# Kernel tuning notes

Measured on AMD Instinct MI355X. Metric: run time of the kernel, lower is better.

Reference implementation:

```python
import jax, jax.numpy as jnp
import numpy as np

T, D, H, P, HEADS, EC = 16, 192, 128, 128, 4, 32  # EC = proj_dim // 4
HD = P // HEADS  # head dim = 32


def setup_inputs() -> dict:
    key = jax.random.key(0)
    ks = jax.random.split(key, 16)
    def nrm(k, shp, s=0.02):
        return jax.random.normal(k, shp, jnp.float32) * s
    x = jax.random.normal(ks[0], (T, H, D), jnp.float32)
    u = jax.random.uniform(ks[1], (D, D))
    w = jax.random.uniform(ks[2], (D, D))
    edge_w = jnp.where(u < 0.05, w, 0.0)
    return dict(
        x=x, edge_w=edge_w,
        W_node=nrm(ks[3], (H, P)), b_node=jnp.zeros(P),
        W_edge=nrm(ks[4], (1, EC)), b_edge=jnp.zeros(EC),
        time_enc=nrm(ks[5], (P,)),
        Wqkv=nrm(ks[6], (P, 3 * P)), bqkv=jnp.zeros(3 * P),
        Wo=nrm(ks[7], (P, P)), bo=jnp.zeros(P),
        W1=nrm(ks[8], (P, 4 * P)), b1=jnp.zeros(4 * P),
        W2=nrm(ks[9], (4 * P, P)), b2=jnp.zeros(P),
        g1=jnp.ones(P), beta1=jnp.zeros(P), g2=jnp.ones(P), beta2=jnp.zeros(P),
        Wc1=nrm(ks[10], (2 * P + EC, P)), bc1=jnp.zeros(P),
        Wc2=nrm(ks[11], (P, 1)), bc2=jnp.zeros(1),
        Wd1=nrm(ks[12], (2 * P, P)), bd1=jnp.zeros(P),
        Wd2=nrm(ks[13], (P, 1)), bd2=jnp.zeros(1),
    )


def _ln(z, g, b):
    m = z.mean(-1, keepdims=True)
    v = ((z - m) ** 2).mean(-1, keepdims=True)
    return (z - m) / jnp.sqrt(v + 1e-5) * g + b


def _heads(t, S):
    return t.reshape(S, HEADS, HD).transpose(1, 0, 2)  # (h, S, hd)


def _forward(x, edge_w, W_node, b_node, W_edge, b_edge, time_enc, Wqkv, bqkv,
             Wo, bo, W1, b1, W2, b2, g1, beta1, g2, beta2,
             Wc1, bc1, Wc2, bc2, Wd1, bd1, Wd2, bd2):
    S = T * D
    # node encoder: (T,H,D) -> (T,D,H) -> (T*D,H) -> (T*D,P), dropout is eval-mode identity
    xf = x.transpose(0, 2, 1).reshape(S, H)
    h = jax.nn.relu(xf @ W_node + b_node)
    # learned time encoding scaled by time index
    t_idx = jnp.repeat(jnp.arange(T, dtype=jnp.float32), D)
    h = h + time_enc[None, :] * t_idx[:, None]
    # spatiotemporal mask: attend to self+neighbors at t and t-1 (vectorized kron)
    adj = (edge_w > 0) | jnp.eye(D, dtype=bool)
    time_allow = jnp.eye(T, dtype=bool) | jnp.eye(T, k=-1, dtype=bool)
    allow = (time_allow[:, None, :, None] & adj[None, :, None, :]).reshape(S, S)
    scale = 1.0 / np.sqrt(HD)
    z = h
    for _ in range(2):  # num_layers=2, shared weights as in the source
        y = _ln(z, g1, beta1)
        qkv = y @ Wqkv + bqkv
        q, k, v = jnp.split(qkv, 3, axis=-1)
        scores = jnp.einsum('hqd,hkd->hqk', _heads(q, S), _heads(k, S)) * scale
        scores = jnp.where(allow[None], scores, -jnp.inf)
        a = jax.nn.softmax(scores, axis=-1)
        attn = jnp.einsum('hqk,hkd->hqd', a, _heads(v, S))
        z = z + attn.transpose(1, 0, 2).reshape(S, P) @ Wo + bo
        y = _ln(z, g2, beta2)
        z = z + jax.nn.relu(y @ W1 + b1) @ W2 + b2
    nf = z.reshape(T, D, P)
    curr, nxt = nf[:-1], nf[1:]  # (T-1, D, P)
    # edge encoder: Linear(1->EC)+ReLU on edge weights
    edge_enc = jax.nn.relu(edge_w[:, :, None] * W_edge[0] + b_edge)  # (D, D, EC)
    # update classifier on concat[next_i, curr_j, edge] -> split the first matmul
    hn = nxt @ Wc1[:P]            # (T-1, D, P)
    hc = curr @ Wc1[P:2 * P]      # (T-1, D, P)
    he = edge_enc @ Wc1[2 * P:]   # (D, D, P)
    hcls = jax.nn.relu(hn[:, :, None, :] + hc[:, None, :, :] + he[None] + bc1)
    logits = (hcls @ Wc2)[..., 0] + bc2[0]  # (T-1, D, D)
    mask = (edge_w == 0) & ~jnp.eye(D, dtype=bool)
    logits = jnp.where(mask[None], -1e9, logits)
    # distance predictor on concat[curr, next]
    hd = jax.nn.relu(curr @ Wd1[:P] + nxt @ Wd1[P:] + bd1)
    dist = (hd @ Wd2)[..., 0] + bd2[0]  # (T-1, D)
    return logits, dist


def reference(x, edge_w, W_node, b_node, W_edge, b_edge, time_enc, Wqkv, bqkv,
              Wo, bo, W1, b1, W2, b2, g1, beta1, g2, beta2,
              Wc1, bc1, Wc2, bc2, Wd1, bd1, Wd2, bd2):
    return _forward(x, edge_w, W_node, b_node, W_edge, b_edge, time_enc, Wqkv,
                    bqkv, Wo, bo, W1, b1, W2, b2, g1, beta1, g2, beta2,
                    Wc1, bc1, Wc2, bc2, Wd1, bd1, Wd2, bd2)
```

## Files before the change

kernel.cpp:

```cpp
#include <hip/hip_runtime.h>
#include <hip/hip_bf16.h>

constexpr int T_ = 16;
constexpr int D_ = 192;
constexpr int H_ = 128;
constexpr int P_ = 128;
constexpr int HEADS_ = 4;
constexpr int HD_ = 32;
constexpr int EC_ = 32;
constexpr int S_ = T_ * D_;
constexpr int FF_ = 512;
constexpr float SCALE_ = 0.17677669529663687f;

__global__ __launch_bounds__(64) void adj_kernel(const float* __restrict__ edge_w,
                                                 int* __restrict__ adj_cnt,
                                                 int* __restrict__ adj_list) {
  int i = blockIdx.x;
  int lane = threadIdx.x;
  int cnt = 0;
  for (int base = 0; base < D_; base += 64) {
    int j = base + lane;
    bool pred = (edge_w[i * D_ + j] > 0.f) || (j == i);
    unsigned long long mb = __ballot(pred);
    int ofs = __popcll(mb & ((1ull << lane) - 1ull));
    if (pred) adj_list[i * D_ + cnt + ofs] = j;
    cnt += __popcll(mb);
  }
  if (lane == 0) adj_cnt[i] = cnt;
}

__global__ __launch_bounds__(128) void node_embed_kernel(
    const float* __restrict__ x, const float* __restrict__ W_node,
    const float* __restrict__ b_node, const float* __restrict__ time_enc,
    float* __restrict__ z) {
  int s0 = blockIdx.x * 8;
  int j = threadIdx.x;
  __shared__ float As[8 * H_];
  for (int idx = j; idx < 8 * H_; idx += 128) {
    int r = idx >> 7;
    int h = idx & 127;
    int s = s0 + r;
    int t = s / D_;
    int d = s - t * D_;
    As[idx] = x[(t * H_ + h) * D_ + d];
  }
  __syncthreads();
  float acc[8];
  float bj = b_node[j];
#pragma unroll
  for (int r = 0; r < 8; ++r) acc[r] = bj;
  for (int h = 0; h < H_; h += 4) {
    float4 w;
    w.x = W_node[(h + 0) * P_ + j];
    w.y = W_node[(h + 1) * P_ + j];
    w.z = W_node[(h + 2) * P_ + j];
    w.w = W_node[(h + 3) * P_ + j];
#pragma unroll
    for (int r = 0; r < 8; ++r) {
      const float4 a = *reinterpret_cast<const float4*>(&As[r * H_ + h]);
      acc[r] = fmaf(a.x, w.x, acc[r]);
      acc[r] = fmaf(a.y, w.y, acc[r]);
      acc[r] = fmaf(a.z, w.z, acc[r]);
      acc[r] = fmaf(a.w, w.w, acc[r]);
    }
  }
  float te = time_enc[j];
#pragma unroll
  for (int r = 0; r < 8; ++r) {
    int s = s0 + r;
    int t = s / D_;
    z[s * P_ + j] = fmaxf(acc[r], 0.f) + te * (float)t;
  }
}

template <int K, int N, int NT, int BM, bool RELU, bool ACCUM, bool BIAS, bool LN>
__global__ __launch_bounds__(NT) void gemm2_k(
    const float* __restrict__ A, const float* __restrict__ B,
    const float* __restrict__ bias, const float* __restrict__ lng,
    const float* __restrict__ lnb, float* __restrict__ C) {
  constexpr int CPT = N / NT;
  int m0 = blockIdx.x * BM;
  int tid = threadIdx.x;
  __shared__ float As[BM * K];
  {
    float4* As4 = reinterpret_cast<float4*>(As);
    const float4* A4 = reinterpret_cast<const float4*>(A + (size_t)m0 * K);
    for (int idx = tid; idx < BM * K / 4; idx += NT) As4[idx] = A4[idx];
  }
  __syncthreads();
  if (LN) {
    static_assert(!LN || K == 128, "LN requires K==128");
    int wv = tid >> 6, lane = tid & 63;
    constexpr int NW = NT / 64;
    for (int r = wv; r < BM; r += NW) {
      float v0 = As[r * K + lane], v1 = As[r * K + 64 + lane];
      float s = v0 + v1;
#pragma unroll
      for (int m = 1; m < 64; m <<= 1) s += __shfl_xor(s, m);
      float mean = s * (1.f / 128.f);
      float d0 = v0 - mean, d1 = v1 - mean;
      float q = d0 * d0 + d1 * d1;
#pragma unroll
      for (int m = 1; m < 64; m <<= 1) q += __shfl_xor(q, m);
      float inv = 1.f / sqrtf(q * (1.f / 128.f) + 1e-5f);
      As[r * K + lane] = d0 * inv * lng[lane] + lnb[lane];
      As[r * K + 64 + lane] = d1 * inv * lng[lane + 64] + lnb[lane + 64];
    }
    __syncthreads();
  }

  if (CPT == 2) {
    int c0 = 2 * tid;
    float acc0[BM], acc1[BM];
    float b0 = BIAS ? bias[c0] : 0.f;
    float b1 = BIAS ? bias[c0 + 1] : 0.f;
#pragma unroll
    for (int r = 0; r < BM; ++r) {
      acc0[r] = b0;
      acc1[r] = b1;
    }
    for (int k = 0; k < K; k += 4) {
      float2 bv0 = *reinterpret_cast<const float2*>(B + (size_t)(k + 0) * N + c0);
      float2 bv1 = *reinterpret_cast<const float2*>(B + (size_t)(k + 1) * N + c0);
      float2 bv2 = *reinterpret_cast<const float2*>(B + (size_t)(k + 2) * N + c0);
      float2 bv3 = *reinterpret_cast<const float2*>(B + (size_t)(k + 3) * N + c0);
#pragma unroll
      for (int r = 0; r < BM; ++r) {
        const float4 a = *reinterpret_cast<const float4*>(&As[r * K + k]);
        acc0[r] = fmaf(a.x, bv0.x, acc0[r]);
        acc1[r] = fmaf(a.x, bv0.y, acc1[r]);
        acc0[r] = fmaf(a.y, bv1.x, acc0[r]);
        acc1[r] = fmaf(a.y, bv1.y, acc1[r]);
        acc0[r] = fmaf(a.z, bv2.x, acc0[r]);
        acc1[r] = fmaf(a.z, bv2.y, acc1[r]);
        acc0[r] = fmaf(a.w, bv3.x, acc0[r]);
        acc1[r] = fmaf(a.w, bv3.y, acc1[r]);
      }
    }
#pragma unroll
    for (int r = 0; r < BM; ++r) {
      float v0 = acc0[r], v1 = acc1[r];
      if (RELU) {
        v0 = fmaxf(v0, 0.f);
        v1 = fmaxf(v1, 0.f);
      }
      float* cp = C + (size_t)(m0 + r) * N + c0;
      if (ACCUM) {
        float2 old = *reinterpret_cast<float2*>(cp);
        old.x += v0;
        old.y += v1;
        *reinterpret_cast<float2*>(cp) = old;
      } else {
        float2 nv;
        nv.x = v0;
        nv.y = v1;
        *reinterpret_cast<float2*>(cp) = nv;
      }
    }
  } else {
    int j = tid;
    float acc[BM];
    float bj = BIAS ? bias[j] : 0.f;
#pragma unroll
    for (int r = 0; r < BM; ++r) acc[r] = bj;
    for (int k = 0; k < K; k += 4) {
      float b0 = B[(size_t)(k + 0) * N + j];
      float b1 = B[(size_t)(k + 1) * N + j];
      float b2 = B[(size_t)(k + 2) * N + j];
      float b3 = B[(size_t)(k + 3) * N + j];
#pragma unroll
      for (int r = 0; r < BM; ++r) {
        const float4 a = *reinterpret_cast<const float4*>(&As[r * K + k]);
        acc[r] = fmaf(a.x, b0, acc[r]);
        acc[r] = fmaf(a.y, b1, acc[r]);
        acc[r] = fmaf(a.z, b2, acc[r]);
        acc[r] = fmaf(a.w, b3, acc[r]);
      }
    }
#pragma unroll
    for (int r = 0; r < BM; ++r) {
      float v = acc[r];
      if (RELU) v = fmaxf(v, 0.f);
      float* cp = C + (size_t)(m0 + r) * N + j;
      if (ACCUM)
        *cp += v;
      else
        *cp = v;
    }
  }
}

__global__ __launch_bounds__(256) void pre_gemm_kernel(
    const float* __restrict__ A, const float* __restrict__ Wc1,
    const float* __restrict__ Wd1, float* __restrict__ pre) {
  constexpr int K = 128, N = 512, NT = 256, BM = 8;
  int m0 = blockIdx.x * BM;
  int tid = threadIdx.x;
  __shared__ float As[BM * K];
  {
    float4* As4 = reinterpret_cast<float4*>(As);
    const float4* A4 = reinterpret_cast<const float4*>(A + (size_t)m0 * K);
    for (int idx = tid; idx < BM * K / 4; idx += NT) As4[idx] = A4[idx];
  }
  __syncthreads();
  int c0 = 2 * tid;
  int seg = c0 >> 7;
  int cc = c0 & 127;
  const float* Bbase = (seg < 2 ? Wc1 : Wd1) + ((seg & 1) ? 128 * P_ : 0) + cc;
  float acc0[BM], acc1[BM];
#pragma unroll
  for (int r = 0; r < BM; ++r) {
    acc0[r] = 0.f;
    acc1[r] = 0.f;
  }
  for (int k = 0; k < K; k += 4) {
    float2 bv0 = *reinterpret_cast<const float2*>(Bbase + (size_t)(k + 0) * P_);
    float2 bv1 = *reinterpret_cast<const float2*>(Bbase + (size_t)(k + 1) * P_);
    float2 bv2 = *reinterpret_cast<const float2*>(Bbase + (size_t)(k + 2) * P_);
    float2 bv3 = *reinterpret_cast<const float2*>(Bbase + (size_t)(k + 3) * P_);
#pragma unroll
    for (int r = 0; r < BM; ++r) {
      const float4 a = *reinterpret_cast<const float4*>(&As[r * K + k]);
      acc0[r] = fmaf(a.x, bv0.x, acc0[r]);
      acc1[r] = fmaf(a.x, bv0.y, acc1[r]);
      acc0[r] = fmaf(a.y, bv1.x, acc0[r]);
      acc1[r] = fmaf(a.y, bv1.y, acc1[r]);
      acc0[r] = fmaf(a.z, bv2.x, acc0[r]);
      acc1[r] = fmaf(a.z, bv2.y, acc1[r]);
      acc0[r] = fmaf(a.w, bv3.x, acc0[r]);
      acc1[r] = fmaf(a.w, bv3.y, acc1[r]);
    }
  }
#pragma unroll
  for (int r = 0; r < BM; ++r) {
    float2 nv;
    nv.x = acc0[r];
    nv.y = acc1[r];
    *reinterpret_cast<float2*>(pre + (size_t)(m0 + r) * N + c0) = nv;
  }
}

__global__ __launch_bounds__(128) void attn_kernel(
    const float* __restrict__ qkv, const int* __restrict__ adj_cnt,
    const int* __restrict__ adj_list, float* __restrict__ out) {
  int s = blockIdx.x;
  int t = s / D_, d1 = s - t * D_;
  int tid = threadIdx.x;
  __shared__ int klist[D_];
  __shared__ float scores[HEADS_][2 * D_];

  int nd2 = adj_cnt[d1];
  for (int kd = tid; kd < nd2; kd += 128) klist[kd] = adj_list[d1 * D_ + kd];
  __syncthreads();
  int t0 = (t > 0) ? t - 1 : 0;
  int ntp = (t > 0) ? 2 : 1;
  int nk = nd2 * ntp;

  float q = qkv[s * 384 + tid];
  int h = tid >> 5, dd = tid & 31;

  for (int tp = 0; tp < ntp; ++tp) {
    int tt = t0 + tp;
    for (int kd = 0; kd < nd2; ++kd) {
      int sk = tt * D_ + klist[kd];
      float partial = q * qkv[sk * 384 + P_ + tid];
      partial += __shfl_xor(partial, 1);
      partial += __shfl_xor(partial, 2);
      partial += __shfl_xor(partial, 4);
      partial += __shfl_xor(partial, 8);
      partial += __shfl_xor(partial, 16);
      if (dd == 0) scores[h][tp * nd2 + kd] = partial * SCALE_;
    }
  }
  __syncthreads();

  float mx = -1e30f;
  for (int ki = dd; ki < nk; ki += 32) mx = fmaxf(mx, scores[h][ki]);
  mx = fmaxf(mx, __shfl_xor(mx, 1));
  mx = fmaxf(mx, __shfl_xor(mx, 2));
  mx = fmaxf(mx, __shfl_xor(mx, 4));
  mx = fmaxf(mx, __shfl_xor(mx, 8));
  mx = fmaxf(mx, __shfl_xor(mx, 16));
  float ssum = 0.f;
  for (int ki = dd; ki < nk; ki += 32) {
    float e = expf(scores[h][ki] - mx);
    scores[h][ki] = e;
    ssum += e;
  }
  ssum += __shfl_xor(ssum, 1);
  ssum += __shfl_xor(ssum, 2);
  ssum += __shfl_xor(ssum, 4);
  ssum += __shfl_xor(ssum, 8);
  ssum += __shfl_xor(ssum, 16);
  float inv = 1.f / ssum;
  __syncthreads();

  float acc = 0.f;
  for (int tp = 0; tp < ntp; ++tp) {
    int tt = t0 + tp;
    for (int kd = 0; kd < nd2; ++kd) {
      float aev = scores[h][tp * nd2 + kd];
      int sk = tt * D_ + klist[kd];
      acc = fmaf(aev, qkv[sk * 384 + 2 * P_ + tid], acc);
    }
  }
  out[s * P_ + tid] = acc * inv;
}

__global__ __launch_bounds__(64) void logits_kernel(
    const float* __restrict__ pre, const int* __restrict__ adj_cnt,
    const int* __restrict__ adj_list, const float* __restrict__ edge_w,
    const float* __restrict__ W_edge, const float* __restrict__ b_edge,
    const float* __restrict__ Wc1e, const float* __restrict__ bc1,
    const float* __restrict__ Wc2, const float* __restrict__ bc2,
    float* __restrict__ logits) {
  int i = blockIdx.x;
  int t = blockIdx.y;
  int lane = threadIdx.x;
  float* lrow = logits + (size_t)(t * D_ + i) * D_;
  for (int j = lane; j < D_; j += 64) lrow[j] = -1e9f;

  const float* hnr = pre + (size_t)((t + 1) * D_ + i) * 512;
  float hn0 = hnr[lane], hn1 = hnr[lane + 64];
  float bc1_0 = bc1[lane], bc1_1 = bc1[lane + 64];
  float wc0 = Wc2[lane], wc1 = Wc2[lane + 64];
  float bb = bc2[0];
  int cnt = adj_cnt[i];
  for (int jj = 0; jj < cnt; ++jj) {
    int j = adj_list[i * D_ + jj];
    float w = edge_w[i * D_ + j];
    float he0 = 0.f, he1 = 0.f;
#pragma unroll 8
    for (int e = 0; e < EC_; ++e) {
      float enc = fmaxf(fmaf(w, W_edge[e], b_edge[e]), 0.f);
      he0 = fmaf(enc, Wc1e[e * P_ + lane], he0);
      he1 = fmaf(enc, Wc1e[e * P_ + lane + 64], he1);
    }
    const float* hcr = pre + (size_t)(t * D_ + j) * 512 + 128;
    float sacc = fmaxf(hn0 + hcr[lane] + he0 + bc1_0, 0.f) * wc0 +
                 fmaxf(hn1 + hcr[lane + 64] + he1 + bc1_1, 0.f) * wc1;
#pragma unroll
    for (int m = 1; m < 64; m <<= 1) sacc += __shfl_xor(sacc, m);
    if (lane == 0) lrow[j] = sacc + bb;
  }
}

__global__ __launch_bounds__(256) void dist_kernel(
    const float* __restrict__ pre, const float* __restrict__ bd1,
    const float* __restrict__ Wd2, const float* __restrict__ bd2,
    float* __restrict__ dist) {
  int row = blockIdx.x * 4 + (threadIdx.x >> 6);
  int lane = threadIdx.x & 63;
  const float* a = pre + (size_t)row * 512 + 256;
  const float* b = pre + (size_t)(row + D_) * 512 + 384;
  float v0 = fmaxf(a[lane] + b[lane] + bd1[lane], 0.f) * Wd2[lane];
  float v1 = fmaxf(a[lane + 64] + b[lane + 64] + bd1[lane + 64], 0.f) * Wd2[lane + 64];
  float s = v0 + v1;
#pragma unroll
  for (int m = 1; m < 64; m <<= 1) s += __shfl_xor(s, m);
  if (lane == 0) dist[row] = s + bd2[0];
}

extern "C" void kernel_launch(void* const* d_in, const int* in_sizes, int n_in,
                              void* d_out, int out_size, void* d_ws,
                              size_t ws_size, hipStream_t stream) {
  const float* x = (const float*)d_in[0];
  const float* edge_w = (const float*)d_in[1];
  const float* W_node = (const float*)d_in[2];
  const float* b_node = (const float*)d_in[3];
  const float* W_edge = (const float*)d_in[4];
  const float* b_edge = (const float*)d_in[5];
  const float* time_enc = (const float*)d_in[6];
  const float* Wqkv = (const float*)d_in[7];
  const float* bqkv = (const float*)d_in[8];
  const float* Wo = (const float*)d_in[9];
  const float* bo = (const float*)d_in[10];
  const float* W1 = (const float*)d_in[11];
  const float* b1 = (const float*)d_in[12];
  const float* W2 = (const float*)d_in[13];
  const float* b2 = (const float*)d_in[14];
  const float* g1 = (const float*)d_in[15];
  const float* beta1 = (const float*)d_in[16];
  const float* g2 = (const float*)d_in[17];
  const float* beta2 = (const float*)d_in[18];
  const float* Wc1 = (const float*)d_in[19];
  const float* bc1 = (const float*)d_in[20];
  const float* Wc2 = (const float*)d_in[21];
  const float* bc2 = (const float*)d_in[22];
  const float* Wd1 = (const float*)d_in[23];
  const float* bd1 = (const float*)d_in[24];
  const float* Wd2 = (const float*)d_in[25];
  const float* bd2 = (const float*)d_in[26];

  float* ws = (float*)d_ws;
  float* qkvb = ws;
  float* attnout = qkvb + S_ * 3 * P_;
  float* mid = attnout + S_ * P_;
  float* z = mid + S_ * FF_;
  int* adj_cnt = (int*)(z + S_ * P_);
  int* adj_list = adj_cnt + D_;
  float* pre = mid;

  float* logits = (float*)d_out;
  float* dist = (float*)d_out + (T_ - 1) * D_ * D_;

  adj_kernel<<<D_, 64, 0, stream>>>(edge_w, adj_cnt, adj_list);
  node_embed_kernel<<<S_ / 8, 128, 0, stream>>>(x, W_node, b_node, time_enc, z);

  for (int it = 0; it < 2; ++it) {
    gemm2_k<128, 384, 192, 8, false, false, true, true>
        <<<S_ / 8, 192, 0, stream>>>(z, Wqkv, bqkv, g1, beta1, qkvb);
    attn_kernel<<<S_, 128, 0, stream>>>(qkvb, adj_cnt, adj_list, attnout);
    gemm2_k<128, 128, 128, 8, false, true, true, false>
        <<<S_ / 8, 128, 0, stream>>>(attnout, Wo, bo, nullptr, nullptr, z);
    gemm2_k<128, 512, 256, 8, true, false, true, true>
        <<<S_ / 8, 256, 0, stream>>>(z, W1, b1, g2, beta2, mid);
    gemm2_k<512, 128, 128, 8, false, true, true, false>
        <<<S_ / 8, 128, 0, stream>>>(mid, W2, b2, nullptr, nullptr, z);
  }

  pre_gemm_kernel<<<S_ / 8, 256, 0, stream>>>(z, Wc1, Wd1, pre);

  logits_kernel<<<dim3(D_, T_ - 1), 64, 0, stream>>>(
      pre, adj_cnt, adj_list, edge_w, W_edge, b_edge, Wc1 + 2 * P_ * P_, bc1,
      Wc2, bc2, logits);
  dist_kernel<<<(T_ - 1) * D_ / 4, 256, 0, stream>>>(pre, bd1, Wd2, bd2, dist);
}
```

Baseline: 356.1 us.

## Fuse transformer layer stages into fewer kernels and drop intermediate buffers

The adjacency build is folded into the node-embedding kernel, and the Wo projection plus residual add into the attention kernel. The two FFN matmuls become one kernel that keeps the hidden activations in shared memory, and the dist head is merged into the logits kernel. The QKV kernel now processes 16 rows per block, and two barriers in attention are removed because each head's scores are produced and consumed by lanes of one wavefront. The goal is fewer launches and less global-memory traffic for attnout and mid. In exchange, the Wo projection now runs one row per block with little weight reuse, and the large shared-memory footprint of the FFN kernel may lower occupancy.

```diff
diff --git a/kernel.cpp b/kernel.cpp
--- a/kernel.cpp
+++ b/kernel.cpp
@@ -1,226 +1,116 @@
 #include <hip/hip_runtime.h>
-#include <hip/hip_bf16.h>
 
 constexpr int T_ = 16;
 constexpr int D_ = 192;
 constexpr int H_ = 128;
 constexpr int P_ = 128;
-constexpr int HEADS_ = 4;
-constexpr int HD_ = 32;
 constexpr int EC_ = 32;
 constexpr int S_ = T_ * D_;
 constexpr int FF_ = 512;
 constexpr float SCALE_ = 0.17677669529663687f;
 
-__global__ __launch_bounds__(64) void adj_kernel(const float* __restrict__ edge_w,
-                                                 int* __restrict__ adj_cnt,
-                                                 int* __restrict__ adj_list) {
-  int i = blockIdx.x;
-  int lane = threadIdx.x;
-  int cnt = 0;
-  for (int base = 0; base < D_; base += 64) {
-    int j = base + lane;
-    bool pred = (edge_w[i * D_ + j] > 0.f) || (j == i);
-    unsigned long long mb = __ballot(pred);
-    int ofs = __popcll(mb & ((1ull << lane) - 1ull));
-    if (pred) adj_list[i * D_ + cnt + ofs] = j;
-    cnt += __popcll(mb);
-  }
-  if (lane == 0) adj_cnt[i] = cnt;
-}
-
-__global__ __launch_bounds__(128) void node_embed_kernel(
+__device__ __forceinline__ float wave_sum64(float v) {
+#pragma unroll
+  for (int m = 1; m < 64; m <<= 1) v += __shfl_xor(v, m);
+  return v;
+}
+
+__global__ __launch_bounds__(128) void embed_adj_kernel(
     const float* __restrict__ x, const float* __restrict__ W_node,
     const float* __restrict__ b_node, const float* __restrict__ time_enc,
-    float* __restrict__ z) {
-  int s0 = blockIdx.x * 8;
-  int j = threadIdx.x;
+    const float* __restrict__ edge_w, float* __restrict__ z,
+    int* __restrict__ adj_cnt, int* __restrict__ adj_list) {
+  int bx = blockIdx.x;
+  int tid = threadIdx.x;
+  if (bx < D_ && tid < 64) {
+    int lane = tid, cnt = 0;
+    for (int base = 0; base < D_; base += 64) {
+      int j = base + lane;
+      bool pred = (edge_w[bx * D_ + j] > 0.f) || (j == bx);
+      unsigned long long mb = __ballot(pred);
+      int ofs = __popcll(mb & ((1ull << lane) - 1ull));
+      if (pred) adj_list[bx * D_ + cnt + ofs] = j;
+      cnt += __popcll(mb);
+    }
+    if (lane == 0) adj_cnt[bx] = cnt;
+  }
   __shared__ float As[8 * H_];
-  for (int idx = j; idx < 8 * H_; idx += 128) {
-    int r = idx >> 7;
-    int h = idx & 127;
-    int s = s0 + r;
-    int t = s / D_;
-    int d = s - t * D_;
+  int m0 = bx * 8;
+  for (int idx = tid; idx < 8 * H_; idx += 128) {
+    int r = idx >> 7, h = idx & 127;
+    int s = m0 + r, t = s / D_, d = s - t * D_;
     As[idx] = x[(t * H_ + h) * D_ + d];
   }
   __syncthreads();
+  int j = tid;
   float acc[8];
   float bj = b_node[j];
 #pragma unroll
   for (int r = 0; r < 8; ++r) acc[r] = bj;
   for (int h = 0; h < H_; h += 4) {
-    float4 w;
-    w.x = W_node[(h + 0) * P_ + j];
-    w.y = W_node[(h + 1) * P_ + j];
-    w.z = W_node[(h + 2) * P_ + j];
-    w.w = W_node[(h + 3) * P_ + j];
+    float w0 = W_node[(h + 0) * P_ + j], w1 = W_node[(h + 1) * P_ + j];
+    float w2 = W_node[(h + 2) * P_ + j], w3 = W_node[(h + 3) * P_ + j];
 #pragma unroll
     for (int r = 0; r < 8; ++r) {
       const float4 a = *reinterpret_cast<const float4*>(&As[r * H_ + h]);
-      acc[r] = fmaf(a.x, w.x, acc[r]);
-      acc[r] = fmaf(a.y, w.y, acc[r]);
-      acc[r] = fmaf(a.z, w.z, acc[r]);
-      acc[r] = fmaf(a.w, w.w, acc[r]);
+      acc[r] = fmaf(a.x, w0, acc[r]);
+      acc[r] = fmaf(a.y, w1, acc[r]);
+      acc[r] = fmaf(a.z, w2, acc[r]);
+      acc[r] = fmaf(a.w, w3, acc[r]);
     }
   }
   float te = time_enc[j];
 #pragma unroll
   for (int r = 0; r < 8; ++r) {
-    int s = s0 + r;
-    int t = s / D_;
-    z[s * P_ + j] = fmaxf(acc[r], 0.f) + te * (float)t;
-  }
-}
-
-template <int K, int N, int NT, int BM, bool RELU, bool ACCUM, bool BIAS, bool LN>
-__global__ __launch_bounds__(NT) void gemm2_k(
-    const float* __restrict__ A, const float* __restrict__ B,
-    const float* __restrict__ bias, const float* __restrict__ lng,
-    const float* __restrict__ lnb, float* __restrict__ C) {
-  constexpr int CPT = N / NT;
+    int s = m0 + r;
+    z[(size_t)s * P_ + j] = fmaxf(acc[r], 0.f) + te * (float)(s / D_);
+  }
+}
+
+__global__ __launch_bounds__(192) void qkv_kernel(
+    const float* __restrict__ z, const float* __restrict__ Wqkv,
+    const float* __restrict__ bqkv, const float* __restrict__ g,
+    const float* __restrict__ b, float* __restrict__ qkvb) {
+  constexpr int BM = 16, NT = 192, N = 384;
   int m0 = blockIdx.x * BM;
   int tid = threadIdx.x;
-  __shared__ float As[BM * K];
-  {
-    float4* As4 = reinterpret_cast<float4*>(As);
-    const float4* A4 = reinterpret_cast<const float4*>(A + (size_t)m0 * K);
-    for (int idx = tid; idx < BM * K / 4; idx += NT) As4[idx] = A4[idx];
-  }
-  __syncthreads();
-  if (LN) {
-    static_assert(!LN || K == 128, "LN requires K==128");
+  __shared__ float As[BM * 128];
+  {
+    float4* As4 = (float4*)As;
+    const float4* Z4 = (const float4*)(z + (size_t)m0 * 128);
+    for (int idx = tid; idx < BM * 32; idx += NT) As4[idx] = Z4[idx];
+  }
+  __syncthreads();
+  {
     int wv = tid >> 6, lane = tid & 63;
-    constexpr int NW = NT / 64;
-    for (int r = wv; r < BM; r += NW) {
-      float v0 = As[r * K + lane], v1 = As[r * K + 64 + lane];
-      float s = v0 + v1;
-#pragma unroll
-      for (int m = 1; m < 64; m <<= 1) s += __shfl_xor(s, m);
+    for (int r = wv; r < BM; r += 3) {
+      float v0 = As[r * 128 + lane], v1 = As[r * 128 + 64 + lane];
+      float s = wave_sum64(v0 + v1);
       float mean = s * (1.f / 128.f);
       float d0 = v0 - mean, d1 = v1 - mean;
-      float q = d0 * d0 + d1 * d1;
-#pragma unroll
-      for (int m = 1; m < 64; m <<= 1) q += __shfl_xor(q, m);
+      float q = wave_sum64(d0 * d0 + d1 * d1);
       float inv = 1.f / sqrtf(q * (1.f / 128.f) + 1e-5f);
-      As[r * K + lane] = d0 * inv * lng[lane] + lnb[lane];
-      As[r * K + 64 + lane] = d1 * inv * lng[lane + 64] + lnb[lane + 64];
-    }
-    __syncthreads();
-  }
-
-  if (CPT == 2) {
-    int c0 = 2 * tid;
-    float acc0[BM], acc1[BM];
-    float b0 = BIAS ? bias[c0] : 0.f;
-    float b1 = BIAS ? bias[c0 + 1] : 0.f;
+      As[r * 128 + lane] = d0 * inv * g[lane] + b[lane];
+      As[r * 128 + 64 + lane] = d1 * inv * g[lane + 64] + b[lane + 64];
+    }
+  }
+  __syncthreads();
+  int c0 = 2 * tid;
+  float acc0[BM], acc1[BM];
+  float b0c = bqkv[c0], b1c = bqkv[c0 + 1];
+#pragma unroll
+  for (int r = 0; r < BM; ++r) {
+    acc0[r] = b0c;
+    acc1[r] = b1c;
+  }
+  for (int k = 0; k < 128; k += 4) {
+    float2 bv0 = *(const float2*)(Wqkv + (size_t)(k + 0) * N + c0);
+    float2 bv1 = *(const float2*)(Wqkv + (size_t)(k + 1) * N + c0);
+    float2 bv2 = *(const float2*)(Wqkv + (size_t)(k + 2) * N + c0);
+    float2 bv3 = *(const float2*)(Wqkv + (size_t)(k + 3) * N + c0);
 #pragma unroll
     for (int r = 0; r < BM; ++r) {
-      acc0[r] = b0;
-      acc1[r] = b1;
-    }
-    for (int k = 0; k < K; k += 4) {
-      float2 bv0 = *reinterpret_cast<const float2*>(B + (size_t)(k + 0) * N + c0);
-      float2 bv1 = *reinterpret_cast<const float2*>(B + (size_t)(k + 1) * N + c0);
-      float2 bv2 = *reinterpret_cast<const float2*>(B + (size_t)(k + 2) * N + c0);
-      float2 bv3 = *reinterpret_cast<const float2*>(B + (size_t)(k + 3) * N + c0);
-#pragma unroll
-      for (int r = 0; r < BM; ++r) {
-        const float4 a = *reinterpret_cast<const float4*>(&As[r * K + k]);
-        acc0[r] = fmaf(a.x, bv0.x, acc0[r]);
-        acc1[r] = fmaf(a.x, bv0.y, acc1[r]);
-        acc0[r] = fmaf(a.y, bv1.x, acc0[r]);
-        acc1[r] = fmaf(a.y, bv1.y, acc1[r]);
-        acc0[r] = fmaf(a.z, bv2.x, acc0[r]);
-        acc1[r] = fmaf(a.z, bv2.y, acc1[r]);
-        acc0[r] = fmaf(a.w, bv3.x, acc0[r]);
-        acc1[r] = fmaf(a.w, bv3.y, acc1[r]);
-      }
-    }
-#pragma unroll
-    for (int r = 0; r < BM; ++r) {
-      float v0 = acc0[r], v1 = acc1[r];
-      if (RELU) {
-        v0 = fmaxf(v0, 0.f);
-        v1 = fmaxf(v1, 0.f);
-      }
-      float* cp = C + (size_t)(m0 + r) * N + c0;
-      if (ACCUM) {
-        float2 old = *reinterpret_cast<float2*>(cp);
-        old.x += v0;
-        old.y += v1;
-        *reinterpret_cast<float2*>(cp) = old;
-      } else {
-        float2 nv;
-        nv.x = v0;
-        nv.y = v1;
-        *reinterpret_cast<float2*>(cp) = nv;
-      }
-    }
-  } else {
-    int j = tid;
-    float acc[BM];
-    float bj = BIAS ? bias[j] : 0.f;
-#pragma unroll
-    for (int r = 0; r < BM; ++r) acc[r] = bj;
-    for (int k = 0; k < K; k += 4) {
-      float b0 = B[(size_t)(k + 0) * N + j];
-      float b1 = B[(size_t)(k + 1) * N + j];
-      float b2 = B[(size_t)(k + 2) * N + j];
-      float b3 = B[(size_t)(k + 3) * N + j];
-#pragma unroll
-      for (int r = 0; r < BM; ++r) {
-        const float4 a = *reinterpret_cast<const float4*>(&As[r * K + k]);
-        acc[r] = fmaf(a.x, b0, acc[r]);
-        acc[r] = fmaf(a.y, b1, acc[r]);
-        acc[r] = fmaf(a.z, b2, acc[r]);
-        acc[r] = fmaf(a.w, b3, acc[r]);
-      }
-    }
-#pragma unroll
-    for (int r = 0; r < BM; ++r) {
-      float v = acc[r];
-      if (RELU) v = fmaxf(v, 0.f);
-      float* cp = C + (size_t)(m0 + r) * N + j;
-      if (ACCUM)
-        *cp += v;
-      else
-        *cp = v;
-    }
-  }
-}
-
-__global__ __launch_bounds__(256) void pre_gemm_kernel(
-    const float* __restrict__ A, const float* __restrict__ Wc1,
-    const float* __restrict__ Wd1, float* __restrict__ pre) {
-  constexpr int K = 128, N = 512, NT = 256, BM = 8;
-  int m0 = blockIdx.x * BM;
-  int tid = threadIdx.x;
-  __shared__ float As[BM * K];
-  {
-    float4* As4 = reinterpret_cast<float4*>(As);
-    const float4* A4 = reinterpret_cast<const float4*>(A + (size_t)m0 * K);
-    for (int idx = tid; idx < BM * K / 4; idx += NT) As4[idx] = A4[idx];
-  }
-  __syncthreads();
-  int c0 = 2 * tid;
-  int seg = c0 >> 7;
-  int cc = c0 & 127;
-  const float* Bbase = (seg < 2 ? Wc1 : Wd1) + ((seg & 1) ? 128 * P_ : 0) + cc;
-  float acc0[BM], acc1[BM];
-#pragma unroll
-  for (int r = 0; r < BM; ++r) {
-    acc0[r] = 0.f;
-    acc1[r] = 0.f;
-  }
-  for (int k = 0; k < K; k += 4) {
-    float2 bv0 = *reinterpret_cast<const float2*>(Bbase + (size_t)(k + 0) * P_);
-    float2 bv1 = *reinterpret_cast<const float2*>(Bbase + (size_t)(k + 1) * P_);
-    float2 bv2 = *reinterpret_cast<const float2*>(Bbase + (size_t)(k + 2) * P_);
-    float2 bv3 = *reinterpret_cast<const float2*>(Bbase + (size_t)(k + 3) * P_);
-#pragma unroll
-    for (int r = 0; r < BM; ++r) {
-      const float4 a = *reinterpret_cast<const float4*>(&As[r * K + k]);
+      const float4 a = *(const float4*)&As[r * 128 + k];
       acc0[r] = fmaf(a.x, bv0.x, acc0[r]);
       acc1[r] = fmaf(a.x, bv0.y, acc1[r]);
       acc0[r] = fmaf(a.y, bv1.x, acc0[r]);
@@ -236,18 +126,20 @@
     float2 nv;
     nv.x = acc0[r];
     nv.y = acc1[r];
-    *reinterpret_cast<float2*>(pre + (size_t)(m0 + r) * N + c0) = nv;
-  }
-}
-
-__global__ __launch_bounds__(128) void attn_kernel(
-    const float* __restrict__ qkv, const int* __restrict__ adj_cnt,
-    const int* __restrict__ adj_list, float* __restrict__ out) {
+    *(float2*)(qkvb + (size_t)(m0 + r) * N + c0) = nv;
+  }
+}
+
+__global__ __launch_bounds__(128) void attn_wo_kernel(
+    const float* __restrict__ qkvb, const int* __restrict__ adj_cnt,
+    const int* __restrict__ adj_list, const float* __restrict__ Wo,
+    const float* __restrict__ bo, float* __restrict__ z) {
   int s = blockIdx.x;
   int t = s / D_, d1 = s - t * D_;
   int tid = threadIdx.x;
   __shared__ int klist[D_];
-  __shared__ float scores[HEADS_][2 * D_];
+  __shared__ float scores[4][2 * D_];
+  __shared__ float att[128];
 
   int nd2 = adj_cnt[d1];
   for (int kd = tid; kd < nd2; kd += 128) klist[kd] = adj_list[d1 * D_ + kd];
@@ -256,14 +148,14 @@
   int ntp = (t > 0) ? 2 : 1;
   int nk = nd2 * ntp;
 
-  float q = qkv[s * 384 + tid];
+  float q = qkvb[(size_t)s * 384 + tid];
   int h = tid >> 5, dd = tid & 31;
 
   for (int tp = 0; tp < ntp; ++tp) {
     int tt = t0 + tp;
     for (int kd = 0; kd < nd2; ++kd) {
       int sk = tt * D_ + klist[kd];
-      float partial = q * qkv[sk * 384 + P_ + tid];
+      float partial = q * qkvb[(size_t)sk * 384 + P_ + tid];
       partial += __shfl_xor(partial, 1);
       partial += __shfl_xor(partial, 2);
       partial += __shfl_xor(partial, 4);
@@ -272,8 +164,6 @@
       if (dd == 0) scores[h][tp * nd2 + kd] = partial * SCALE_;
     }
   }
-  __syncthreads();
-
   float mx = -1e30f;
   for (int ki = dd; ki < nk; ki += 32) mx = fmaxf(mx, scores[h][ki]);
   mx = fmaxf(mx, __shfl_xor(mx, 1));
@@ -293,7 +183,6 @@
   ssum += __shfl_xor(ssum, 8);
   ssum += __shfl_xor(ssum, 16);
   float inv = 1.f / ssum;
-  __syncthreads();
 
   float acc = 0.f;
   for (int tp = 0; tp < ntp; ++tp) {
@@ -301,23 +190,176 @@
     for (int kd = 0; kd < nd2; ++kd) {
       float aev = scores[h][tp * nd2 + kd];
       int sk = tt * D_ + klist[kd];
-      acc = fmaf(aev, qkv[sk * 384 + 2 * P_ + tid], acc);
-    }
-  }
-  out[s * P_ + tid] = acc * inv;
-}
-
-__global__ __launch_bounds__(64) void logits_kernel(
+      acc = fmaf(aev, qkvb[(size_t)sk * 384 + 2 * P_ + tid], acc);
+    }
+  }
+  att[tid] = acc * inv;
+  __syncthreads();
+
+  int c = tid;
+  float p = 0.f;
+  for (int k = 0; k < 128; k += 4) {
+    const float4 a = *(const float4*)&att[k];
+    p = fmaf(a.x, Wo[(size_t)(k + 0) * P_ + c], p);
+    p = fmaf(a.y, Wo[(size_t)(k + 1) * P_ + c], p);
+    p = fmaf(a.z, Wo[(size_t)(k + 2) * P_ + c], p);
+    p = fmaf(a.w, Wo[(size_t)(k + 3) * P_ + c], p);
+  }
+  z[(size_t)s * P_ + c] += p + bo[c];
+}
+
+__global__ __launch_bounds__(256) void ffn_kernel(
+    const float* __restrict__ zin, const float* __restrict__ W1,
+    const float* __restrict__ b1, const float* __restrict__ W2,
+    const float* __restrict__ b2, const float* __restrict__ g,
+    const float* __restrict__ b, float* __restrict__ z) {
+  constexpr int BM = 8, NT = 256;
+  int m0 = blockIdx.x * BM;
+  int tid = threadIdx.x;
+  __shared__ float As[BM * 128];
+  __shared__ float mid[BM * FF_];
+  {
+    float4* As4 = (float4*)As;
+    const float4* Z4 = (const float4*)(zin + (size_t)m0 * 128);
+    for (int idx = tid; idx < BM * 32; idx += NT) As4[idx] = Z4[idx];
+  }
+  __syncthreads();
+  {
+    int wv = tid >> 6, lane = tid & 63;
+    for (int r = wv; r < BM; r += 4) {
+      float v0 = As[r * 128 + lane], v1 = As[r * 128 + 64 + lane];
+      float s = wave_sum64(v0 + v1);
+      float mean = s * (1.f / 128.f);
+      float d0 = v0 - mean, d1 = v1 - mean;
+      float qv = wave_sum64(d0 * d0 + d1 * d1);
+      float inv = 1.f / sqrtf(qv * (1.f / 128.f) + 1e-5f);
+      As[r * 128 + lane] = d0 * inv * g[lane] + b[lane];
+      As[r * 128 + 64 + lane] = d1 * inv * g[lane + 64] + b[lane + 64];
+    }
+  }
+  __syncthreads();
+  {
+    int c0 = 2 * tid;
+    float acc0[BM], acc1[BM];
+    float bb0 = b1[c0], bb1 = b1[c0 + 1];
+#pragma unroll
+    for (int r = 0; r < BM; ++r) {
+      acc0[r] = bb0;
+      acc1[r] = bb1;
+    }
+    for (int k = 0; k < 128; k += 4) {
+      float2 bv0 = *(const float2*)(W1 + (size_t)(k + 0) * FF_ + c0);
+      float2 bv1 = *(const float2*)(W1 + (size_t)(k + 1) * FF_ + c0);
+      float2 bv2 = *(const float2*)(W1 + (size_t)(k + 2) * FF_ + c0);
+      float2 bv3 = *(const float2*)(W1 + (size_t)(k + 3) * FF_ + c0);
+#pragma unroll
+      for (int r = 0; r < BM; ++r) {
+        const float4 a = *(const float4*)&As[r * 128 + k];
+        acc0[r] = fmaf(a.x, bv0.x, acc0[r]);
+        acc1[r] = fmaf(a.x, bv0.y, acc1[r]);
+        acc0[r] = fmaf(a.y, bv1.x, acc0[r]);
+        acc1[r] = fmaf(a.y, bv1.y, acc1[r]);
+        acc0[r] = fmaf(a.z, bv2.x, acc0[r]);
+        acc1[r] = fmaf(a.z, bv2.y, acc1[r]);
+        acc0[r] = fmaf(a.w, bv3.x, acc0[r]);
+        acc1[r] = fmaf(a.w, bv3.y, acc1[r]);
+      }
+    }
+#pragma unroll
+    for (int r = 0; r < BM; ++r) {
+      mid[r * FF_ + c0] = fmaxf(acc0[r], 0.f);
+      mid[r * FF_ + c0 + 1] = fmaxf(acc1[r], 0.f);
+    }
+  }
+  __syncthreads();
+  {
+    int rg = tid >> 7, col = tid & 127;
+    int r0 = rg * 4;
+    float acc[4] = {0.f, 0.f, 0.f, 0.f};
+    for (int k = 0; k < FF_; k += 4) {
+      float w0 = W2[(size_t)(k + 0) * P_ + col];
+      float w1 = W2[(size_t)(k + 1) * P_ + col];
+      float w2 = W2[(size_t)(k + 2) * P_ + col];
+      float w3 = W2[(size_t)(k + 3) * P_ + col];
+#pragma unroll
+      for (int i = 0; i < 4; ++i) {
+        const float4 a = *(const float4*)&mid[(r0 + i) * FF_ + k];
+        acc[i] = fmaf(a.x, w0, acc[i]);
+        acc[i] = fmaf(a.y, w1, acc[i]);
+        acc[i] = fmaf(a.z, w2, acc[i]);
+        acc[i] = fmaf(a.w, w3, acc[i]);
+      }
+    }
+    float bb = b2[col];
+#pragma unroll
+    for (int i = 0; i < 4; ++i)
+      z[(size_t)(m0 + r0 + i) * P_ + col] += acc[i] + bb;
+  }
+}
+
+__global__ __launch_bounds__(256) void pre_gemm_kernel(
+    const float* __restrict__ A, const float* __restrict__ Wc1,
+    const float* __restrict__ Wd1, float* __restrict__ pre) {
+  constexpr int K = 128, N = 512, NT = 256, BM = 8;
+  int m0 = blockIdx.x * BM;
+  int tid = threadIdx.x;
+  __shared__ float As[BM * K];
+  {
+    float4* As4 = (float4*)As;
+    const float4* A4 = (const float4*)(A + (size_t)m0 * K);
+    for (int idx = tid; idx < BM * K / 4; idx += NT) As4[idx] = A4[idx];
+  }
+  __syncthreads();
+  int c0 = 2 * tid;
+  int seg = c0 >> 7, cc = c0 & 127;
+  const float* Bbase = (seg < 2 ? Wc1 : Wd1) + ((seg & 1) ? P_ * P_ : 0) + cc;
+  float acc0[BM], acc1[BM];
+#pragma unroll
+  for (int r = 0; r < BM; ++r) {
+    acc0[r] = 0.f;
+    acc1[r] = 0.f;
+  }
+  for (int k = 0; k < K; k += 4) {
+    float2 bv0 = *(const float2*)(Bbase + (size_t)(k + 0) * P_);
+    float2 bv1 = *(const float2*)(Bbase + (size_t)(k + 1) * P_);
+    float2 bv2 = *(const float2*)(Bbase + (size_t)(k + 2) * P_);
+    float2 bv3 = *(const float2*)(Bbase + (size_t)(k + 3) * P_);
+#pragma unroll
+    for (int r = 0; r < BM; ++r) {
+      const float4 a = *(const float4*)&As[r * K + k];
+      acc0[r] = fmaf(a.x, bv0.x, acc0[r]);
+      acc1[r] = fmaf(a.x, bv0.y, acc1[r]);
+      acc0[r] = fmaf(a.y, bv1.x, acc0[r]);
+      acc1[r] = fmaf(a.y, bv1.y, acc1[r]);
+      acc0[r] = fmaf(a.z, bv2.x, acc0[r]);
+      acc1[r] = fmaf(a.z, bv2.y, acc1[r]);
+      acc0[r] = fmaf(a.w, bv3.x, acc0[r]);
+      acc1[r] = fmaf(a.w, bv3.y, acc1[r]);
+    }
+  }
+#pragma unroll
+  for (int r = 0; r < BM; ++r) {
+    float2 nv;
+    nv.x = acc0[r];
+    nv.y = acc1[r];
+    *(float2*)(pre + (size_t)(m0 + r) * N + c0) = nv;
+  }
+}
+
+__global__ __launch_bounds__(64) void logits_dist_kernel(
     const float* __restrict__ pre, const int* __restrict__ adj_cnt,
     const int* __restrict__ adj_list, const float* __restrict__ edge_w,
     const float* __restrict__ W_edge, const float* __restrict__ b_edge,
     const float* __restrict__ Wc1e, const float* __restrict__ bc1,
     const float* __restrict__ Wc2, const float* __restrict__ bc2,
-    float* __restrict__ logits) {
+    const float* __restrict__ bd1, const float* __restrict__ Wd2,
+    const float* __restrict__ bd2, float* __restrict__ logits,
+    float* __restrict__ dist) {
   int i = blockIdx.x;
   int t = blockIdx.y;
   int lane = threadIdx.x;
-  float* lrow = logits + (size_t)(t * D_ + i) * D_;
+  int w = t * D_ + i;
+  float* lrow = logits + (size_t)w * D_;
   for (int j = lane; j < D_; j += 64) lrow[j] = -1e9f;
 
   const float* hnr = pre + (size_t)((t + 1) * D_ + i) * 512;
@@ -328,37 +370,27 @@
   int cnt = adj_cnt[i];
   for (int jj = 0; jj < cnt; ++jj) {
     int j = adj_list[i * D_ + jj];
-    float w = edge_w[i * D_ + j];
+    float wv = edge_w[i * D_ + j];
     float he0 = 0.f, he1 = 0.f;
 #pragma unroll 8
     for (int e = 0; e < EC_; ++e) {
-      float enc = fmaxf(fmaf(w, W_edge[e], b_edge[e]), 0.f);
+      float enc = fmaxf(fmaf(wv, W_edge[e], b_edge[e]), 0.f);
       he0 = fmaf(enc, Wc1e[e * P_ + lane], he0);
       he1 = fmaf(enc, Wc1e[e * P_ + lane + 64], he1);
     }
     const float* hcr = pre + (size_t)(t * D_ + j) * 512 + 128;
     float sacc = fmaxf(hn0 + hcr[lane] + he0 + bc1_0, 0.f) * wc0 +
                  fmaxf(hn1 + hcr[lane + 64] + he1 + bc1_1, 0.f) * wc1;
-#pragma unroll
-    for (int m = 1; m < 64; m <<= 1) sacc += __shfl_xor(sacc, m);
+    sacc = wave_sum64(sacc);
     if (lane == 0) lrow[j] = sacc + bb;
   }
-}
-
-__global__ __launch_bounds__(256) void dist_kernel(
-    const float* __restrict__ pre, const float* __restrict__ bd1,
-    const float* __restrict__ Wd2, const float* __restrict__ bd2,
-    float* __restrict__ dist) {
-  int row = blockIdx.x * 4 + (threadIdx.x >> 6);
-  int lane = threadIdx.x & 63;
-  const float* a = pre + (size_t)row * 512 + 256;
-  const float* b = pre + (size_t)(row + D_) * 512 + 384;
-  float v0 = fmaxf(a[lane] + b[lane] + bd1[lane], 0.f) * Wd2[lane];
-  float v1 = fmaxf(a[lane + 64] + b[lane + 64] + bd1[lane + 64], 0.f) * Wd2[lane + 64];
-  float s = v0 + v1;
-#pragma unroll
-  for (int m = 1; m < 64; m <<= 1) s += __shfl_xor(s, m);
-  if (lane == 0) dist[row] = s + bd2[0];
+
+  const float* ar = pre + (size_t)w * 512 + 256;
+  const float* br = pre + (size_t)(w + D_) * 512 + 384;
+  float v0 = fmaxf(ar[lane] + br[lane] + bd1[lane], 0.f) * Wd2[lane];
+  float v1 = fmaxf(ar[lane + 64] + br[lane + 64] + bd1[lane + 64], 0.f) * Wd2[lane + 64];
+  float sd = wave_sum64(v0 + v1);
+  if (lane == 0) dist[w] = sd + bd2[0];
 }
 
 extern "C" void kernel_launch(void* const* d_in, const int* in_sizes, int n_in,
@@ -393,36 +425,24 @@
   const float* bd2 = (const float*)d_in[26];
 
   float* ws = (float*)d_ws;
-  float* qkvb = ws;
-  float* attnout = qkvb + S_ * 3 * P_;
-  float* mid = attnout + S_ * P_;
-  float* z = mid + S_ * FF_;
-  int* adj_cnt = (int*)(z + S_ * P_);
+  float* z = ws;
+  float* qkvb = z + S_ * 128;
+  float* pre = qkvb + S_ * 384;
+  int* adj_cnt = (int*)(pre + S_ * 512);
   int* adj_list = adj_cnt + D_;
-  float* pre = mid;
 
   float* logits = (float*)d_out;
   float* dist = (float*)d_out + (T_ - 1) * D_ * D_;
 
-  adj_kernel<<<D_, 64, 0, stream>>>(edge_w, adj_cnt, adj_list);
-  node_embed_kernel<<<S_ / 8, 128, 0, stream>>>(x, W_node, b_node, time_enc, z);
-
+  embed_adj_kernel<<<S_ / 8, 128, 0, stream>>>(x, W_node, b_node, time_enc,
+                                               edge_w, z, adj_cnt, adj_list);
   for (int it = 0; it < 2; ++it) {
-    gemm2_k<128, 384, 192, 8, false, false, true, true>
-        <<<S_ / 8, 192, 0, stream>>>(z, Wqkv, bqkv, g1, beta1, qkvb);
-    attn_kernel<<<S_, 128, 0, stream>>>(qkvb, adj_cnt, adj_list, attnout);
-    gemm2_k<128, 128, 128, 8, false, true, true, false>
-        <<<S_ / 8, 128, 0, stream>>>(attnout, Wo, bo, nullptr, nullptr, z);
-    gemm2_k<128, 512, 256, 8, true, false, true, true>
-        <<<S_ / 8, 256, 0, stream>>>(z, W1, b1, g2, beta2, mid);
-    gemm2_k<512, 128, 128, 8, false, true, true, false>
-        <<<S_ / 8, 128, 0, stream>>>(mid, W2, b2, nullptr, nullptr, z);
-  }
-
+    qkv_kernel<<<S_ / 16, 192, 0, stream>>>(z, Wqkv, bqkv, g1, beta1, qkvb);
+    attn_wo_kernel<<<S_, 128, 0, stream>>>(qkvb, adj_cnt, adj_list, Wo, bo, z);
+    ffn_kernel<<<S_ / 8, 256, 0, stream>>>(z, W1, b1, W2, b2, g2, beta2, z);
+  }
   pre_gemm_kernel<<<S_ / 8, 256, 0, stream>>>(z, Wc1, Wd1, pre);
-
-  logits_kernel<<<dim3(D_, T_ - 1), 64, 0, stream>>>(
+  logits_dist_kernel<<<dim3(D_, T_ - 1), 64, 0, stream>>>(
       pre, adj_cnt, adj_list, edge_w, W_edge, b_edge, Wc1 + 2 * P_ * P_, bc1,
-      Wc2, bc2, logits);
-  dist_kernel<<<(T_ - 1) * D_ / 4, 256, 0, stream>>>(pre, bd1, Wd2, bd2, dist);
-}
+      Wc2, bc2, bd1, Wd2, bd2, logits, dist);
+}
```

After: 326.1 us. 8.4% less time.
